# Optimization experiments

Hardware: AMD Instinct MI355X
Metric: run time of the kernel (lower is better)

Reference implementation:

```python
import jax, jax.numpy as jnp
import numpy as np


def setup_inputs() -> dict:
    key = jax.random.key(0)
    ks = jax.random.split(key, 6)
    B, V, C, T = 32, 2048, 64, 64
    x = jax.random.normal(ks[0], (B, V, C, T), dtype=jnp.float32)
    U_1 = jax.random.normal(ks[1], (V,), dtype=jnp.float32)
    U_2 = jax.random.normal(ks[2], (C, V), dtype=jnp.float32)
    U_3 = jax.random.normal(ks[3], (C,), dtype=jnp.float32)
    b_e = jax.random.normal(ks[4], (1, T, T), dtype=jnp.float32)
    V_e = jax.random.normal(ks[5], (B, T, T), dtype=jnp.float32)
    return {"x": x, "U_1": U_1, "U_2": U_2, "U_3": U_3, "b_e": b_e, "V_e": V_e}


def reference(x, U_1, U_2, U_3, b_e, V_e):
    # x: (B, V, C, T)
    # lhs = (x^T . U_1) . U_2  -> (B, T, V)
    lhs = jnp.einsum('bvct,v->btc', x, U_1) @ U_2          # (B,T,C) @ (C,V) -> (B,T,V)
    # rhs = x^T . U_3 -> (B, V, T)
    rhs = jnp.einsum('bvct,c->bvt', x, U_3)                # (B,V,T)
    product = jnp.einsum('btv,bvu->btu', lhs, rhs)          # (B,T,T)
    # E = V_e @ sigmoid(product + b_e); V_e broadcast over batch
    E = jnp.einsum('bts,bsu->btu', V_e, jax.nn.sigmoid(product + b_e))  # (B,T,T)
    # manual softmax along dim 1 (shift-invariant -> equivalent to jax.nn.softmax)
    return jax.nn.softmax(E, axis=1)
```

## Files before the change

kernel.cpp:

```cpp
#include <hip/hip_runtime.h>
#include <math.h>

#define NB 32
#define NV 2048
#define NC 64
#define NT 64
#define VC 32
#define CHUNKS (NV / VC)

__global__ __launch_bounds__(256) void k1_pass_x(
    const float* __restrict__ x,
    const float* __restrict__ U1,
    const float* __restrict__ U2,
    const float* __restrict__ U3,
    float* __restrict__ part)
{
    const int tid = threadIdx.x;
    const int blk = blockIdx.x;
    const int b     = blk / CHUNKS;
    const int chunk = blk % CHUNKS;
    const int v0    = chunk * VC;

    const int w     = tid >> 6;
    const int l     = tid & 63;
    const int u0    = w * 16 + (l & 3) * 4;
    const int cbase = l >> 2;

    __shared__ float U2s[VC][NC];

    for (int i = tid; i < VC * NC; i += 256) {
        const int c  = i >> 5;
        const int vi = i & 31;
        U2s[vi][c] = U2[c * NV + v0 + vi];
    }

    float u3r[4];
#pragma unroll
    for (int k = 0; k < 4; ++k) u3r[k] = U3[cbase + 16 * k];

    float4 t1r[4], mr[4];
#pragma unroll
    for (int k = 0; k < 4; ++k) {
        t1r[k] = make_float4(0.f, 0.f, 0.f, 0.f);
        mr[k]  = make_float4(0.f, 0.f, 0.f, 0.f);
    }

    __syncthreads();

    const float* xb = x + (size_t)(b * NV + v0) * NC * NT + u0;

#pragma unroll 4
    for (int vi = 0; vi < VC; ++vi) {
        const float* xv = xb + (size_t)vi * NC * NT;

        float4 xa[4];
#pragma unroll
        for (int k = 0; k < 4; ++k)
            xa[k] = *reinterpret_cast<const float4*>(xv + (cbase + 16 * k) * NT);

        const float u1v = U1[v0 + vi];

        float4 rh = make_float4(0.f, 0.f, 0.f, 0.f);
#pragma unroll
        for (int k = 0; k < 4; ++k) {
            t1r[k].x = fmaf(u1v, xa[k].x, t1r[k].x);
            t1r[k].y = fmaf(u1v, xa[k].y, t1r[k].y);
            t1r[k].z = fmaf(u1v, xa[k].z, t1r[k].z);
            t1r[k].w = fmaf(u1v, xa[k].w, t1r[k].w);
            rh.x = fmaf(u3r[k], xa[k].x, rh.x);
            rh.y = fmaf(u3r[k], xa[k].y, rh.y);
            rh.z = fmaf(u3r[k], xa[k].z, rh.z);
            rh.w = fmaf(u3r[k], xa[k].w, rh.w);
        }

#pragma unroll
        for (int m = 4; m <= 32; m <<= 1) {
            rh.x += __shfl_xor(rh.x, m, 64);
            rh.y += __shfl_xor(rh.y, m, 64);
            rh.z += __shfl_xor(rh.z, m, 64);
            rh.w += __shfl_xor(rh.w, m, 64);
        }

#pragma unroll
        for (int k = 0; k < 4; ++k) {
            const float u2v = U2s[vi][cbase + 16 * k];
            mr[k].x = fmaf(u2v, rh.x, mr[k].x);
            mr[k].y = fmaf(u2v, rh.y, mr[k].y);
            mr[k].z = fmaf(u2v, rh.z, mr[k].z);
            mr[k].w = fmaf(u2v, rh.w, mr[k].w);
        }
    }

    float* pb = part + (size_t)(b * CHUNKS + chunk) * 2 * NC * NT;
#pragma unroll
    for (int k = 0; k < 4; ++k) {
        const int off = (cbase + 16 * k) * NT + u0;
        *reinterpret_cast<float4*>(&pb[off])           = t1r[k];
        *reinterpret_cast<float4*>(&pb[NC * NT + off]) = mr[k];
    }
}

__global__ __launch_bounds__(256) void k2a_reduce(
    const float4* __restrict__ part4,
    float4* __restrict__ fin4)
{
    const int j = blockIdx.x;
    const int b = j >> 3;
    const int local = (j & 7) * 256 + threadIdx.x;

    const float4* p = part4 + (size_t)b * CHUNKS * 2048 + local;
    float4 acc = make_float4(0.f, 0.f, 0.f, 0.f);
#pragma unroll 8
    for (int ch = 0; ch < CHUNKS; ++ch) {
        const float4 v = p[(size_t)ch * 2048];
        acc.x += v.x; acc.y += v.y; acc.z += v.z; acc.w += v.w;
    }
    fin4[(size_t)b * 2048 + local] = acc;
}

__global__ __launch_bounds__(256) void k2b_epilogue(
    const float* __restrict__ fin,
    const float* __restrict__ b_e,
    const float* __restrict__ V_e,
    float* __restrict__ out)
{
    const int b = blockIdx.x;
    const int tid = threadIdx.x;

    __shared__ float t1[NC * NT];
    __shared__ float Mb[NC * NT];
    __shared__ float P[NT * NT];
    __shared__ float Eb[NT * NT];

    const float* t1g = fin + (size_t)b * 2 * NC * NT;
    const float* mgb = t1g + NC * NT;
    for (int i = tid * 4; i < NC * NT; i += 1024) {
        *reinterpret_cast<float4*>(&t1[i]) = *reinterpret_cast<const float4*>(&t1g[i]);
        *reinterpret_cast<float4*>(&Mb[i]) = *reinterpret_cast<const float4*>(&mgb[i]);
    }
    __syncthreads();

    const int u  = tid & 63;
    const int tg = tid >> 6;

    for (int i = 0; i < 16; ++i) {
        const int t = tg * 16 + i;
        float acc = 0.f;
#pragma unroll 8
        for (int c = 0; c < NC; ++c)
            acc = fmaf(t1[c * NT + t], Mb[c * NT + u], acc);
        const float z = acc + b_e[t * NT + u];
        P[t * NT + u] = 1.0f / (1.0f + expf(-z));
    }
    __syncthreads();

    const float* veb = V_e + (size_t)b * NT * NT;
    for (int i = 0; i < 16; ++i) {
        const int t = tg * 16 + i;
        float acc = 0.f;
#pragma unroll 8
        for (int s = 0; s < NT; ++s)
            acc = fmaf(veb[t * NT + s], P[s * NT + u], acc);
        Eb[t * NT + u] = acc;
    }
    __syncthreads();

    if (tid < NT) {
        const int uu = tid;
        float m = -INFINITY;
        for (int t = 0; t < NT; ++t) m = fmaxf(m, Eb[t * NT + uu]);
        float ssum = 0.f;
        for (int t = 0; t < NT; ++t) {
            const float e = expf(Eb[t * NT + uu] - m);
            Eb[t * NT + uu] = e;
            ssum += e;
        }
        const float inv = 1.0f / ssum;
        for (int t = 0; t < NT; ++t)
            out[(size_t)b * NT * NT + t * NT + uu] = Eb[t * NT + uu] * inv;
    }
}

extern "C" void kernel_launch(void* const* d_in, const int* in_sizes, int n_in,
                              void* d_out, int out_size, void* d_ws, size_t ws_size,
                              hipStream_t stream) {
    const float* x   = (const float*)d_in[0];
    const float* U1  = (const float*)d_in[1];
    const float* U2  = (const float*)d_in[2];
    const float* U3  = (const float*)d_in[3];
    const float* b_e = (const float*)d_in[4];
    const float* V_e = (const float*)d_in[5];
    float* out = (float*)d_out;

    float* part = (float*)d_ws;
    float* fin  = part + (size_t)NB * CHUNKS * 2 * NC * NT;

    k1_pass_x<<<NB * CHUNKS, 256, 0, stream>>>(x, U1, U2, U3, part);
    k2a_reduce<<<256, 256, 0, stream>>>((const float4*)part, (float4*)fin);
    k2b_epilogue<<<NB, 256, 0, stream>>>(fin, b_e, V_e, out);
}
```

Baseline: 306.2 us.

## Widen V chunk, remap threads to full T rows, reduce M via shared memory

Doubles the V chunk per block, which halves the number of partial tiles written and later reduced. Threads are remapped so each wave covers all 64 T columns for a group of C rows. This cuts the shuffle reduction of rh to two steps, and each thread now accumulates 16 M outputs from float4 U2 loads out of a padded shared buffer. The per-wave M partials are then summed through shared memory with serialized syncs. The reduce kernel gets four independent accumulators. The trade-offs are 64 float4 accumulators in registers, which lowers occupancy, and a serialized shared-memory merge.

```diff
diff --git a/kernel.cpp b/kernel.cpp
--- a/kernel.cpp
+++ b/kernel.cpp
@@ -5,8 +5,9 @@
 #define NV 2048
 #define NC 64
 #define NT 64
-#define VC 32
+#define VC 64
 #define CHUNKS (NV / VC)
+#define U2P 68
 
 __global__ __launch_bounds__(256) void k1_pass_x(
     const float* __restrict__ x,
@@ -21,42 +22,42 @@
     const int chunk = blk % CHUNKS;
     const int v0    = chunk * VC;
 
-    const int w     = tid >> 6;
-    const int l     = tid & 63;
-    const int u0    = w * 16 + (l & 3) * 4;
-    const int cbase = l >> 2;
-
-    __shared__ float U2s[VC][NC];
+    const int w    = tid >> 6;
+    const int l    = tid & 63;
+    const int u0   = (l & 15) * 4;
+    const int crow = l >> 4;
+    const int cw   = w * 16 + crow;
+
+    __shared__ float U2s[VC][U2P];
+    __shared__ float Msum[NC * NT];
 
     for (int i = tid; i < VC * NC; i += 256) {
-        const int c  = i >> 5;
-        const int vi = i & 31;
+        const int c  = i >> 6;
+        const int vi = i & 63;
         U2s[vi][c] = U2[c * NV + v0 + vi];
     }
 
     float u3r[4];
 #pragma unroll
-    for (int k = 0; k < 4; ++k) u3r[k] = U3[cbase + 16 * k];
-
-    float4 t1r[4], mr[4];
-#pragma unroll
-    for (int k = 0; k < 4; ++k) {
-        t1r[k] = make_float4(0.f, 0.f, 0.f, 0.f);
-        mr[k]  = make_float4(0.f, 0.f, 0.f, 0.f);
-    }
-
-    __syncthreads();
-
-    const float* xb = x + (size_t)(b * NV + v0) * NC * NT + u0;
-
-#pragma unroll 4
+    for (int k = 0; k < 4; ++k) u3r[k] = U3[cw + 4 * k];
+
+    float4 t1r[4], mr[16];
+#pragma unroll
+    for (int k = 0; k < 4; ++k) t1r[k] = make_float4(0.f, 0.f, 0.f, 0.f);
+#pragma unroll
+    for (int j = 0; j < 16; ++j) mr[j] = make_float4(0.f, 0.f, 0.f, 0.f);
+
+    __syncthreads();
+
+    const float* xb = x + (size_t)(b * NV + v0) * (NC * NT) + cw * NT + u0;
+
     for (int vi = 0; vi < VC; ++vi) {
-        const float* xv = xb + (size_t)vi * NC * NT;
+        const float* xv = xb + (size_t)vi * (NC * NT);
 
         float4 xa[4];
 #pragma unroll
         for (int k = 0; k < 4; ++k)
-            xa[k] = *reinterpret_cast<const float4*>(xv + (cbase + 16 * k) * NT);
+            xa[k] = *reinterpret_cast<const float4*>(xv + 4 * k * NT);
 
         const float u1v = U1[v0 + vi];
 
@@ -74,7 +75,7 @@
         }
 
 #pragma unroll
-        for (int m = 4; m <= 32; m <<= 1) {
+        for (int m = 16; m <= 32; m <<= 1) {
             rh.x += __shfl_xor(rh.x, m, 64);
             rh.y += __shfl_xor(rh.y, m, 64);
             rh.z += __shfl_xor(rh.z, m, 64);
@@ -82,22 +83,54 @@
         }
 
 #pragma unroll
-        for (int k = 0; k < 4; ++k) {
-            const float u2v = U2s[vi][cbase + 16 * k];
-            mr[k].x = fmaf(u2v, rh.x, mr[k].x);
-            mr[k].y = fmaf(u2v, rh.y, mr[k].y);
-            mr[k].z = fmaf(u2v, rh.z, mr[k].z);
-            mr[k].w = fmaf(u2v, rh.w, mr[k].w);
+        for (int j4 = 0; j4 < 4; ++j4) {
+            const float4 u2v = *reinterpret_cast<const float4*>(
+                &U2s[vi][crow * 16 + 4 * j4]);
+            mr[4 * j4 + 0].x = fmaf(u2v.x, rh.x, mr[4 * j4 + 0].x);
+            mr[4 * j4 + 0].y = fmaf(u2v.x, rh.y, mr[4 * j4 + 0].y);
+            mr[4 * j4 + 0].z = fmaf(u2v.x, rh.z, mr[4 * j4 + 0].z);
+            mr[4 * j4 + 0].w = fmaf(u2v.x, rh.w, mr[4 * j4 + 0].w);
+            mr[4 * j4 + 1].x = fmaf(u2v.y, rh.x, mr[4 * j4 + 1].x);
+            mr[4 * j4 + 1].y = fmaf(u2v.y, rh.y, mr[4 * j4 + 1].y);
+            mr[4 * j4 + 1].z = fmaf(u2v.y, rh.z, mr[4 * j4 + 1].z);
+            mr[4 * j4 + 1].w = fmaf(u2v.y, rh.w, mr[4 * j4 + 1].w);
+            mr[4 * j4 + 2].x = fmaf(u2v.z, rh.x, mr[4 * j4 + 2].x);
+            mr[4 * j4 + 2].y = fmaf(u2v.z, rh.y, mr[4 * j4 + 2].y);
+            mr[4 * j4 + 2].z = fmaf(u2v.z, rh.z, mr[4 * j4 + 2].z);
+            mr[4 * j4 + 2].w = fmaf(u2v.z, rh.w, mr[4 * j4 + 2].w);
+            mr[4 * j4 + 3].x = fmaf(u2v.w, rh.x, mr[4 * j4 + 3].x);
+            mr[4 * j4 + 3].y = fmaf(u2v.w, rh.y, mr[4 * j4 + 3].y);
+            mr[4 * j4 + 3].z = fmaf(u2v.w, rh.z, mr[4 * j4 + 3].z);
+            mr[4 * j4 + 3].w = fmaf(u2v.w, rh.w, mr[4 * j4 + 3].w);
         }
     }
 
     float* pb = part + (size_t)(b * CHUNKS + chunk) * 2 * NC * NT;
-#pragma unroll
-    for (int k = 0; k < 4; ++k) {
-        const int off = (cbase + 16 * k) * NT + u0;
-        *reinterpret_cast<float4*>(&pb[off])           = t1r[k];
-        *reinterpret_cast<float4*>(&pb[NC * NT + off]) = mr[k];
-    }
+
+#pragma unroll
+    for (int k = 0; k < 4; ++k)
+        *reinterpret_cast<float4*>(&pb[(cw + 4 * k) * NT + u0]) = t1r[k];
+
+    for (int i = 0; i < 4; ++i) {
+        if (w == i) {
+#pragma unroll
+            for (int j = 0; j < 16; ++j) {
+                float* d = &Msum[(crow * 16 + j) * NT + u0];
+                if (i == 0) {
+                    *reinterpret_cast<float4*>(d) = mr[j];
+                } else {
+                    d[0] += mr[j].x; d[1] += mr[j].y;
+                    d[2] += mr[j].z; d[3] += mr[j].w;
+                }
+            }
+        }
+        __syncthreads();
+    }
+
+    float* pbM = pb + NC * NT;
+    for (int i = tid * 4; i < NC * NT; i += 1024)
+        *reinterpret_cast<float4*>(&pbM[i]) =
+            *reinterpret_cast<const float4*>(&Msum[i]);
 }
 
 __global__ __launch_bounds__(256) void k2a_reduce(
@@ -109,12 +142,24 @@
     const int local = (j & 7) * 256 + threadIdx.x;
 
     const float4* p = part4 + (size_t)b * CHUNKS * 2048 + local;
-    float4 acc = make_float4(0.f, 0.f, 0.f, 0.f);
-#pragma unroll 8
-    for (int ch = 0; ch < CHUNKS; ++ch) {
-        const float4 v = p[(size_t)ch * 2048];
-        acc.x += v.x; acc.y += v.y; acc.z += v.z; acc.w += v.w;
-    }
+    float4 a0 = make_float4(0.f, 0.f, 0.f, 0.f);
+    float4 a1 = a0, a2 = a0, a3 = a0;
+#pragma unroll
+    for (int ch = 0; ch < CHUNKS; ch += 4) {
+        const float4 v0 = p[(size_t)(ch + 0) * 2048];
+        const float4 v1 = p[(size_t)(ch + 1) * 2048];
+        const float4 v2 = p[(size_t)(ch + 2) * 2048];
+        const float4 v3 = p[(size_t)(ch + 3) * 2048];
+        a0.x += v0.x; a0.y += v0.y; a0.z += v0.z; a0.w += v0.w;
+        a1.x += v1.x; a1.y += v1.y; a1.z += v1.z; a1.w += v1.w;
+        a2.x += v2.x; a2.y += v2.y; a2.z += v2.z; a2.w += v2.w;
+        a3.x += v3.x; a3.y += v3.y; a3.z += v3.z; a3.w += v3.w;
+    }
+    float4 acc;
+    acc.x = (a0.x + a1.x) + (a2.x + a3.x);
+    acc.y = (a0.y + a1.y) + (a2.y + a3.y);
+    acc.z = (a0.z + a1.z) + (a2.z + a3.z);
+    acc.w = (a0.w + a1.w) + (a2.w + a3.w);
     fin4[(size_t)b * 2048 + local] = acc;
 }
 
```

After: 257.2 us. -16.0%, faster.
